# Kernel tuning notes

Measured on AMD Instinct MI355X. Metric: run time of the kernel, lower is better.

## Reference

```python
import jax, jax.numpy as jnp
import numpy as np

V, E, T, H, NT, B = 30000, 300, 256, 256, 9, 128


def setup_inputs() -> dict:
    key = jax.random.key(0)
    ks = jax.random.split(key, 12)
    s = 0.05
    # token ids with trailing zero padding (0 = pad), lens in [T//2, T]
    lens = jax.random.randint(ks[0], (B,), T // 2, T + 1)
    tokens = jax.random.randint(ks[1], (B, T), 1, V)
    pos = jnp.arange(T)[None, :]
    inputs = jnp.where(pos < lens[:, None], tokens, 0)
    labels = jax.random.randint(ks[2], (B, T), 0, NT)
    emb = jax.random.normal(ks[3], (V, E), jnp.float32) * s
    Wf = jax.random.normal(ks[4], (E, 4 * H), jnp.float32) * s
    Uf = jax.random.normal(ks[5], (H, 4 * H), jnp.float32) * s
    bf = jnp.zeros((4 * H,), jnp.float32)
    Wb = jax.random.normal(ks[6], (E, 4 * H), jnp.float32) * s
    Ub = jax.random.normal(ks[7], (H, 4 * H), jnp.float32) * s
    bb = jnp.zeros((4 * H,), jnp.float32)
    fcW = jax.random.normal(ks[8], (2 * H, NT), jnp.float32) * s
    fcb = jnp.zeros((NT,), jnp.float32)
    trans = jax.random.uniform(ks[9], (NT, NT), jnp.float32)  # tf.random.uniform init
    return dict(inputs=inputs, labels=labels, emb=emb, Wf=Wf, Uf=Uf, bf=bf,
                Wb=Wb, Ub=Ub, bb=bb, fcW=fcW, fcb=fcb, trans=trans)


def _lstm(x, W, U, b):
    """Keras LSTM (gate order i,f,g,o). x: [B,T,E] -> [B,T,H]."""
    xW = jnp.einsum('bte,eh->bth', x, W) + b  # precompute input projections

    def step(carry, xt):
        h, c = carry
        z = xt + h @ U
        i, f, g, o = jnp.split(z, 4, axis=-1)
        i = jax.nn.sigmoid(i)
        f = jax.nn.sigmoid(f)
        g = jnp.tanh(g)
        o = jax.nn.sigmoid(o)
        c = f * c + i * g
        h = o * jnp.tanh(c)
        return (h, c), h

    Bq = x.shape[0]
    Hq = U.shape[0]
    init = (jnp.zeros((Bq, Hq), x.dtype), jnp.zeros((Bq, Hq), x.dtype))
    _, hs = jax.lax.scan(step, init, jnp.swapaxes(xW, 0, 1))  # [T,B,H]
    return jnp.swapaxes(hs, 0, 1)


def _crf_log_likelihood(logits, labels, lens, trans):
    """tfa.text.crf_log_likelihood: gold score - log partition. logits: [B,T,N]."""
    Bq, Tq, Nq = logits.shape
    pos = jnp.arange(Tq)[None, :]
    mask = pos < lens[:, None]  # [B,T]
    # unary (emission) score of the gold path
    unary = jnp.take_along_axis(logits, labels[..., None], axis=-1)[..., 0]
    score = jnp.sum(jnp.where(mask, unary, 0.0), axis=-1)
    # binary (transition) score of the gold path
    btrans = trans[labels[:, :-1], labels[:, 1:]]
    bmask = pos[:, 1:] < lens[:, None]
    score = score + jnp.sum(jnp.where(bmask, btrans, 0.0), axis=-1)
    # forward algorithm (log partition) with per-timestep length masking
    def step(alpha, inp):
        logit_t, m_t = inp  # [B,N], [B]
        new = jax.nn.logsumexp(alpha[:, :, None] + trans[None], axis=1) + logit_t
        return jnp.where(m_t[:, None], new, alpha), None

    alpha0 = logits[:, 0]
    xs = (jnp.swapaxes(logits[:, 1:], 0, 1), jnp.swapaxes(mask[:, 1:], 0, 1))
    alpha, _ = jax.lax.scan(step, alpha0, xs)
    log_norm = jax.nn.logsumexp(alpha, axis=-1)
    return score - log_norm


def reference(inputs, labels, emb, Wf, Uf, bf, Wb, Ub, bb, fcW, fcb, trans):
    text_lens = jnp.sum((inputs != 0).astype(jnp.int32), axis=-1)
    x = emb[inputs]  # [B,T,E]
    hf = _lstm(x, Wf, Uf, bf)
    hb = _lstm(x[:, ::-1], Wb, Ub, bb)[:, ::-1]
    h = jnp.concatenate([hf, hb], axis=-1)  # [B,T,2H]
    logits = h @ fcW + fcb  # [B,T,NT]
    log_likelihood = _crf_log_likelihood(logits, labels, text_lens, trans)
    return logits, log_likelihood, text_lens
```

## Files before the change

kernel.cpp:

```cpp
#include <hip/hip_runtime.h>
#include <hip/hip_bf16.h>
#include <stdint.h>

#define Bb 128
#define Tt 256
#define Ee 300
#define EP 320
#define Hh 256
#define G4 1024
#define NTAG 9

typedef __bf16 bf16x8 __attribute__((ext_vector_type(8)));
typedef float f32x4 __attribute__((ext_vector_type(4)));
typedef float f32x2 __attribute__((ext_vector_type(2)));
typedef int i32x8 __attribute__((ext_vector_type(8)));
typedef unsigned short u16;
typedef unsigned int u32;
typedef unsigned char u8;
typedef long i64;

union U4B { uint4 q; bf16x8 v; };

static __device__ __forceinline__ float bf2f(u32 u){
  union { float f; u32 u; } w; w.u = u << 16; return w.f;
}
static __device__ __forceinline__ u16 f2bf(float f){
  union { float f; u32 u; } w; w.f = f;
  u32 x = w.u;
  return (u16)((x + 0x7fffu + ((x >> 16) & 1u)) >> 16);
}
static __device__ __forceinline__ int perm2orig(int c){
  int w = c >> 7, r = c & 127, g = r >> 5, jj = r & 31;
  return g * 256 + w * 32 + jj;
}
static __device__ __forceinline__ float frcp(float x){ return __builtin_amdgcn_rcpf(x); }
static __device__ __forceinline__ float fexp2(float x){
  float r; asm("v_exp_f32 %0, %1" : "=v"(r) : "v"(x)); return r;
}
static __device__ __forceinline__ f32x2 vexp2(f32x2 x){
  f32x2 r; r[0] = fexp2(x[0]); r[1] = fexp2(x[1]); return r;
}
static __device__ __forceinline__ f32x2 vrcp(f32x2 x){
  f32x2 r; r[0] = frcp(x[0]); r[1] = frcp(x[1]); return r;
}
static __device__ __forceinline__ f32x2 vfabs(f32x2 x){
  f32x2 r; r[0] = __builtin_fabsf(x[0]); r[1] = __builtin_fabsf(x[1]); return r;
}
static __device__ __forceinline__ f32x2 vminc(f32x2 x, float c){
  f32x2 r; r[0] = fminf(x[0], c); r[1] = fminf(x[1], c); return r;
}
static __device__ __forceinline__ f32x2 vcps(f32x2 m, f32x2 s){
  f32x2 r; r[0] = __builtin_copysignf(m[0], s[0]);
  r[1] = __builtin_copysignf(m[1], s[1]); return r;
}
static __device__ __forceinline__ void gl_lds16(const void* g, void* l){
  __builtin_amdgcn_global_load_lds((const __attribute__((address_space(1))) u32*)(g),
                                   (__attribute__((address_space(3))) u32*)(l), 16, 0, 0);
}

__global__ void pack_w_k(const float* __restrict__ Wf, const float* __restrict__ Wb,
                         u16* __restrict__ Wpk){
  int idx = blockIdx.x * 256 + threadIdx.x;
  if(idx >= 128 * 10 * 64) return;
  int lane = idx & 63;
  int kk = (idx >> 6) % 10;
  int nt2 = idx / 640;
  int d = nt2 >> 6, ntd = nt2 & 63;
  int oc = perm2orig(ntd * 16 + (lane & 15));
  const float* W = d ? Wb : Wf;
  int k0 = kk * 32 + ((lane >> 4) << 3);
  u16 o[8];
  #pragma unroll
  for(int j = 0; j < 8; ++j){
    int k = k0 + j;
    o[j] = (k < Ee) ? f2bf(W[(size_t)k * G4 + oc]) : (u16)0;
  }
  uint4 q;
  q.x = o[0] | ((u32)o[1] << 16); q.y = o[2] | ((u32)o[3] << 16);
  q.z = o[4] | ((u32)o[5] << 16); q.w = o[6] | ((u32)o[7] << 16);
  *(uint4*)(Wpk + (size_t)idx * 8) = q;
}

__global__ void pack_u_k(const float* __restrict__ Uf, const float* __restrict__ Ub,
                         u8* __restrict__ Upk8){
  int idx = blockIdx.x * 256 + threadIdx.x;
  if(idx >= 2 * 64 * 2 * 64) return;
  int lane = idx & 63;
  int kh = (idx >> 6) & 1;
  int nt = (idx >> 7) & 63;
  int d = idx >> 13;
  int oc = perm2orig(nt * 16 + (lane & 15));
  const float* U = d ? Ub : Uf;
  int k0 = kh * 128 + (lane >> 4) * 32;
  u32 o[8];
  #pragma unroll
  for(int m = 0; m < 8; ++m){
    float v0 = U[(size_t)(k0 + 4 * m + 0) * G4 + oc] * 32.f;
    float v1 = U[(size_t)(k0 + 4 * m + 1) * G4 + oc] * 32.f;
    float v2 = U[(size_t)(k0 + 4 * m + 2) * G4 + oc] * 32.f;
    float v3 = U[(size_t)(k0 + 4 * m + 3) * G4 + oc] * 32.f;
    int pk = __builtin_amdgcn_cvt_pk_fp8_f32(v0, v1, 0, false);
    pk = __builtin_amdgcn_cvt_pk_fp8_f32(v2, v3, pk, true);
    o[m] = (u32)pk;
  }
  uint4* dst = (uint4*)(Upk8 + (size_t)idx * 32);
  dst[0] = (uint4){o[0], o[1], o[2], o[3]};
  dst[1] = (uint4){o[4], o[5], o[6], o[7]};
}

__global__ void pack_b_k(const float* __restrict__ bf_, const float* __restrict__ bb_,
                         float* __restrict__ bperm){
  int c = blockIdx.x * 256 + threadIdx.x;
  if(c >= 2048) return;
  const float* src = (c >> 10) ? bb_ : bf_;
  bperm[c] = src[perm2orig(c & 1023)];
}

__global__ void pack_fcw_k(const float* __restrict__ fcW, u8* __restrict__ fcw8){
  int idx = blockIdx.x * 256 + threadIdx.x;
  if(idx >= 1024) return;
  int lane = idx & 63, kk = idx >> 6;
  int col = lane & 15;
  int k0 = kk * 32 + ((lane >> 4) << 3);
  float v[8];
  #pragma unroll
  for(int j = 0; j < 8; ++j)
    v[j] = (col < NTAG) ? fcW[(size_t)(k0 + j) * NTAG + col] * 256.f : 0.f;
  int lo = __builtin_amdgcn_cvt_pk_fp8_f32(v[0], v[1], 0, false);
  lo = __builtin_amdgcn_cvt_pk_fp8_f32(v[2], v[3], lo, true);
  int hi = __builtin_amdgcn_cvt_pk_fp8_f32(v[4], v[5], 0, false);
  hi = __builtin_amdgcn_cvt_pk_fp8_f32(v[6], v[7], hi, true);
  uint2 q; q.x = (u32)lo; q.y = (u32)hi;
  *(uint2*)(fcw8 + (size_t)idx * 8) = q;
}

__global__ void gather_x_k(const int* __restrict__ inp, const float* __restrict__ emb,
                           u16* __restrict__ xbf){
  int row = blockIdx.x * 2 + (threadIdx.x >> 7);
  int j = threadIdx.x & 127;
  int t = row >> 7, b = row & 127;
  int tok = inp[b * Tt + t];
  u16* dst = xbf + (size_t)row * EP;
  if(j < 75){
    float4 v = *(const float4*)(emb + (size_t)tok * Ee + j * 4);
    u32 lo = f2bf(v.x) | ((u32)f2bf(v.y) << 16);
    u32 hi = f2bf(v.z) | ((u32)f2bf(v.w) << 16);
    *(uint2*)(dst + j * 4) = (uint2){lo, hi};
  } else if(j < 80){
    *(uint2*)(dst + j * 4) = (uint2){0u, 0u};
  }
}

__global__ __launch_bounds__(256, 2) void xw_gemm_k(const u16* __restrict__ xbf,
    const u16* __restrict__ Wpk, const float* __restrict__ bperm,
    u16* __restrict__ xwpk){
  __shared__ uint4 At[512];
  int t = blockIdx.y, nblk = blockIdx.x;
  int tid = threadIdx.x, lane = tid & 63, w = tid >> 6;
  int mh = w >> 1, nh = w & 1;
  f32x4 acc[4][4];
  #pragma unroll
  for(int i = 0; i < 4; ++i)
    #pragma unroll
    for(int j = 0; j < 4; ++j) acc[i][j] = (f32x4){0.f, 0.f, 0.f, 0.f};
  for(int ks = 0; ks < 10; ++ks){
    __syncthreads();
    #pragma unroll
    for(int it = 0; it < 2; ++it){
      int row = it * 64 + w * 16 + (lane >> 2);
      int seg = (lane & 3) ^ (row & 3);
      gl_lds16(xbf + (size_t)(t * 128 + row) * EP + ks * 32 + seg * 8,
               &At[it * 256 + w * 64]);
    }
    asm volatile("s_waitcnt vmcnt(0)" ::: "memory");
    __syncthreads();
    U4B a[4], bv[4];
    #pragma unroll
    for(int m = 0; m < 4; ++m){
      int row = (mh * 4 + m) * 16 + (lane & 15);
      a[m].q = At[row * 4 + ((lane >> 4) ^ (row & 3))];
    }
    #pragma unroll
    for(int n = 0; n < 4; ++n){
      int ntg = nblk * 8 + nh * 4 + n;
      bv[n].q = *(const uint4*)(Wpk + ((size_t)(ntg * 10 + ks) * 64 + lane) * 8);
    }
    #pragma unroll
    for(int m = 0; m < 4; ++m)
      #pragma unroll
      for(int n = 0; n < 4; ++n)
        acc[m][n] = __builtin_amdgcn_mfma_f32_16x16x32_bf16(a[m].v, bv[n].v, acc[m][n], 0, 0, 0);
  }
  #pragma unroll
  for(int m = 0; m < 4; ++m){
    int grp = mh * 4 + m;
    #pragma unroll
    for(int n = 0; n < 4; ++n){
      int ntg = nblk * 8 + nh * 4 + n;
      int d = ntg >> 6, nd = ntg & 63;
      float bias = bperm[ntg * 16 + (lane & 15)];
      u16 h0 = f2bf((acc[m][n][0] + bias) * 512.f), h1 = f2bf((acc[m][n][1] + bias) * 512.f);
      u16 h2 = f2bf((acc[m][n][2] + bias) * 512.f), h3 = f2bf((acc[m][n][3] + bias) * 512.f);
      uint2 p; p.x = h0 | ((u32)h1 << 16); p.y = h2 | ((u32)h3 << 16);
      *(uint2*)(xwpk + ((((size_t)(d * 8 + grp) * Tt + t) * 64 + nd) * 64 + lane) * 4) = p;
    }
  }
}

__global__ __launch_bounds__(512, 2) void lstm_rec_k(const u16* __restrict__ xwpk,
    const u8* __restrict__ Upk8, u8* __restrict__ hseq8){
  __shared__ u32 Hf8[2][1024];
  __shared__ uint2 Xw[2][4096];
  int bid = blockIdx.x;
  int d = bid >> 3, grp = bid & 7;
  int tid = threadIdx.x, lane = tid & 63, w = tid >> 6;
  int arow = lane & 15, r4 = lane >> 4;
  if(w & 1) __builtin_amdgcn_s_setprio(1);

  i32x8 Ureg[8][2];
  const u8* Ub8 = Upk8 + (size_t)d * 262144;
  #pragma unroll
  for(int n = 0; n < 8; ++n)
    #pragma unroll
    for(int kh = 0; kh < 2; ++kh)
      Ureg[n][kh] = *(const i32x8*)(Ub8 + (((size_t)(w * 8 + n) * 2 + kh) * 64 + lane) * 32);
  #pragma unroll
  for(int n = 0; n < 8; ++n)
    #pragma unroll
    for(int kh = 0; kh < 2; ++kh)
      asm volatile("" : "+a"(Ureg[n][kh]));

  Hf8[0][tid] = 0u; Hf8[0][tid + 512] = 0u;
  f32x2 cst2[2][2];
  #pragma unroll
  for(int a = 0; a < 2; ++a)
    #pragma unroll
    for(int p = 0; p < 2; ++p) cst2[a][p] = (f32x2){0.f, 0.f};
  const u16* xwb = xwpk + (size_t)(d * 8 + grp) * Tt * 16384;
  u8* hs_base = hseq8 + (size_t)(d * 8 + grp) * Tt * 4096;
  u32 hf8base = (u32)(uintptr_t)(&Hf8[0][0]);
  u32* hf8u = (u32*)(&Hf8[0][0]);

  const float c1s = -1.44269504f / 512.f;
  const f32x2 C1  = (f32x2){c1s, c1s};
  const f32x2 C2  = (f32x2){2.f * c1s, 2.f * c1s};
  const f32x2 C3  = (f32x2){-2.f * 1.44269504f, -2.f * 1.44269504f};
  const f32x2 ONE = (f32x2){1.f, 1.f};

  {
    int t0 = d ? (Tt - 1) : 0;
    const u16* xwt0 = xwb + (size_t)t0 * 16384;
    #pragma unroll
    for(int j = 0; j < 4; ++j)
      gl_lds16(xwt0 + (w * 8 + 2 * j) * 256 + lane * 8, &Xw[0][w * 512 + 2 * j * 64]);
  }
  asm volatile("s_waitcnt vmcnt(0)" ::: "memory");
  __syncthreads();

  int cur = 0;
  for(int st = 0; st < Tt; ++st){
    int t = d ? (Tt - 1 - st) : st;
    int p = st & 1, c_ = p ^ 1;
    union AFU { i64 dd[4]; i32x8 v; };
    AFU af0, af1;
    u32 av = hf8base + (u32)(p * 4096) + (u32)(r4 * 512 + arow * 8);
    asm volatile("ds_read_b64_tr_b8 %0, %1"             : "=v"(af0.dd[0]) : "v"(av));
    asm volatile("ds_read_b64_tr_b8 %0, %1 offset:128"  : "=v"(af0.dd[1]) : "v"(av));
    asm volatile("ds_read_b64_tr_b8 %0, %1 offset:256"  : "=v"(af0.dd[2]) : "v"(av));
    asm volatile("ds_read_b64_tr_b8 %0, %1 offset:384"  : "=v"(af0.dd[3]) : "v"(av));
    asm volatile("ds_read_b64_tr_b8 %0, %1 offset:2048" : "=v"(af1.dd[0]) : "v"(av));
    asm volatile("ds_read_b64_tr_b8 %0, %1 offset:2176" : "=v"(af1.dd[1]) : "v"(av));
    asm volatile("ds_read_b64_tr_b8 %0, %1 offset:2304" : "=v"(af1.dd[2]) : "v"(av));
    asm volatile("ds_read_b64_tr_b8 %0, %1 offset:2432" : "=v"(af1.dd[3]) : "v"(av));
    asm volatile("s_waitcnt lgkmcnt(0)" ::: "memory");
    __builtin_amdgcn_sched_barrier(0);
    asm volatile("s_waitcnt vmcnt(2)" ::: "memory");
    uint2 xw[8];
    #pragma unroll
    for(int n = 0; n < 8; ++n) xw[n] = Xw[cur][w * 512 + n * 64 + lane];
    {
      int stn = (st + 1 < Tt) ? st + 1 : st;
      int tn = d ? (Tt - 1 - stn) : stn;
      const u16* xwtn = xwb + (size_t)tn * 16384;
      #pragma unroll
      for(int j = 0; j < 4; ++j)
        gl_lds16(xwtn + (w * 8 + 2 * j) * 256 + lane * 8, &Xw[cur ^ 1][w * 512 + 2 * j * 64]);
    }
    __builtin_amdgcn_sched_barrier(0);
    f32x4 acc[8];
    #pragma unroll
    for(int n = 0; n < 8; ++n){
      acc[n][0] = bf2f(xw[n].x & 0xffffu);
      acc[n][1] = bf2f(xw[n].x >> 16);
      acc[n][2] = bf2f(xw[n].y & 0xffffu);
      acc[n][3] = bf2f(xw[n].y >> 16);
    }
    #pragma unroll
    for(int n = 0; n < 8; ++n){
      asm volatile("v_mfma_f32_16x16x128_f8f6f4 %0, %1, %2, %0"
                   : "+v"(acc[n]) : "v"(af0.v), "a"(Ureg[n][0]));
      asm volatile("v_mfma_f32_16x16x128_f8f6f4 %0, %1, %2, %0"
                   : "+v"(acc[n]) : "v"(af1.v), "a"(Ureg[n][1]));
    }
    #pragma unroll
    for(int n1 = 0; n1 < 2; ++n1){
      f32x2 h16[2];
      #pragma unroll
      for(int pq = 0; pq < 2; ++pq){
        f32x2 ai = (f32x2){acc[0 + n1][2 * pq], acc[0 + n1][2 * pq + 1]};
        f32x2 af = (f32x2){acc[2 + n1][2 * pq], acc[2 + n1][2 * pq + 1]};
        f32x2 ag = (f32x2){acc[4 + n1][2 * pq], acc[4 + n1][2 * pq + 1]};
        f32x2 ao = (f32x2){acc[6 + n1][2 * pq], acc[6 + n1][2 * pq + 1]};
        f32x2 ei = vexp2(ai * C1);
        f32x2 ef = vexp2(af * C1);
        f32x2 eo = vexp2(ao * C1);
        f32x2 eg = vexp2(vminc(vfabs(ag), 10240.f) * C2);
        f32x2 ig = vcps(ONE - eg, ag) * vrcp((ONE + ei) * (ONE + eg));
        f32x2 fs = vrcp(ONE + ef);
        f32x2 cc = fs * cst2[n1][pq] + ig;
        cst2[n1][pq] = cc;
        f32x2 ec = vexp2(vminc(vfabs(cc), 20.f) * C3);
        f32x2 hh = vcps(ONE - ec, cc) * vrcp((ONE + eo) * (ONE + ec));
        h16[pq] = hh * (f32x2){16.f, 16.f};
      }
      int pk = __builtin_amdgcn_cvt_pk_fp8_f32(h16[0][0], h16[0][1], 0, false);
      pk = __builtin_amdgcn_cvt_pk_fp8_f32(h16[1][0], h16[1][1], pk, true);
      int unit = w * 32 + n1 * 16 + arow;
      hf8u[c_ * 1024 + unit * 4 + r4] = (u32)pk;
      *(u32*)(hs_base + (size_t)t * 4096 + unit * 16 + r4 * 4) = (u32)pk;
    }
    asm volatile("s_waitcnt lgkmcnt(0)" ::: "memory");
    __builtin_amdgcn_s_barrier();
    cur ^= 1;
  }
}

__global__ __launch_bounds__(256) void logits_k(const u8* __restrict__ hseq8,
    const u8* __restrict__ fcw8, const float* __restrict__ fcb,
    float* __restrict__ out){
  __shared__ u8 Ht[4][8192];
  int widx = threadIdx.x >> 6, lane = threadIdx.x & 63;
  int wid = blockIdx.x * 4 + widx;
  int grp = wid >> 8, t = wid & 255;
  i64 bf[16];
  #pragma unroll
  for(int kk = 0; kk < 16; ++kk)
    bf[kk] = *(const i64*)(fcw8 + ((size_t)kk * 64 + lane) * 8);
  const u8* hf = hseq8 + ((size_t)(0 * 8 + grp) * Tt + t) * 4096;
  const u8* hb = hseq8 + ((size_t)(1 * 8 + grp) * Tt + t) * 4096;
  #pragma unroll
  for(int j = 0; j < 4; ++j){
    gl_lds16(hf + j * 1024 + lane * 16, &Ht[widx][j * 1024]);
    gl_lds16(hb + j * 1024 + lane * 16, &Ht[widx][4096 + j * 1024]);
  }
  asm volatile("s_waitcnt vmcnt(0)" ::: "memory");
  __builtin_amdgcn_sched_barrier(0);
  u32 base = (u32)(uintptr_t)(&Ht[widx][0]) + lane * 8;
  i64 afr[16];
  #pragma unroll
  for(int kk = 0; kk < 16; ++kk){
    u32 a = base + kk * 512;
    asm volatile("ds_read_b64_tr_b8 %0, %1" : "=v"(afr[kk]) : "v"(a));
  }
  asm volatile("s_waitcnt lgkmcnt(0)" ::: "memory");
  __builtin_amdgcn_sched_barrier(0);
  f32x4 acc = (f32x4){0.f, 0.f, 0.f, 0.f};
  #pragma unroll
  for(int kk = 0; kk < 16; ++kk)
    acc = __builtin_amdgcn_mfma_f32_16x16x32_fp8_fp8(afr[kk], bf[kk], acc, 0, 0, 0);
  int tag = lane & 15, r4 = lane >> 4;
  if(tag < NTAG){
    float bb = fcb[tag];
    #pragma unroll
    for(int q = 0; q < 4; ++q){
      int b = grp * 16 + r4 * 4 + q;
      out[((size_t)b * Tt + t) * NTAG + tag] = acc[q] * (1.f / 4096.f) + bb;
    }
  }
}

__global__ __launch_bounds__(64) void crf_k(const int* __restrict__ inp,
    const int* __restrict__ labels, const float* __restrict__ trans,
    const float* __restrict__ logits, float* __restrict__ out){
  int b = blockIdx.x;
  int lane = threadIdx.x;
  int cnt = 0;
  for(int t = lane; t < Tt; t += 64) cnt += (inp[b * Tt + t] != 0) ? 1 : 0;
  #pragma unroll
  for(int off = 32; off >= 1; off >>= 1) cnt += __shfl_xor(cnt, off, 64);
  int len = cnt;
  float sc = 0.f;
  for(int t = lane; t < Tt; t += 64){
    if(t < len){
      int lab = labels[b * Tt + t];
      sc += logits[(size_t)(b * Tt + t) * NTAG + lab];
      if(t >= 1){
        int lp = labels[b * Tt + t - 1];
        sc += trans[lp * NTAG + lab];
      }
    }
  }
  #pragma unroll
  for(int off = 32; off >= 1; off >>= 1) sc += __shfl_xor(sc, off, 64);
  float Tc[NTAG];
  if(lane < NTAG){
    #pragma unroll
    for(int i = 0; i < NTAG; ++i) Tc[i] = trans[i * NTAG + lane];
  }
  float alpha = (lane < NTAG) ? logits[(size_t)(b * Tt) * NTAG + lane] : -3.0e38f;
  for(int t = 1; t < len; ++t){
    float av[NTAG];
    #pragma unroll
    for(int i = 0; i < NTAG; ++i) av[i] = __shfl(alpha, i, 64);
    if(lane < NTAG){
      float m = av[0] + Tc[0];
      #pragma unroll
      for(int i = 1; i < NTAG; ++i) m = fmaxf(m, av[i] + Tc[i]);
      float s = 0.f;
      #pragma unroll
      for(int i = 0; i < NTAG; ++i) s += __expf(av[i] + Tc[i] - m);
      alpha = __logf(s) + m + logits[(size_t)(b * Tt + t) * NTAG + lane];
    }
  }
  float av[NTAG];
  #pragma unroll
  for(int i = 0; i < NTAG; ++i) av[i] = __shfl(alpha, i, 64);
  float m = av[0];
  #pragma unroll
  for(int i = 1; i < NTAG; ++i) m = fmaxf(m, av[i]);
  float s = 0.f;
  #pragma unroll
  for(int i = 0; i < NTAG; ++i) s += __expf(av[i] - m);
  float ln = __logf(s) + m;
  if(lane == 0){
    out[(size_t)Bb * Tt * NTAG + b] = sc - ln;
    out[(size_t)Bb * Tt * NTAG + Bb + b] = (float)len;
  }
}

extern "C" void kernel_launch(void* const* d_in, const int* in_sizes, int n_in,
                              void* d_out, int out_size, void* d_ws, size_t ws_size,
                              hipStream_t stream) {
  const int*   inputs = (const int*)d_in[0];
  const int*   labels = (const int*)d_in[1];
  const float* emb    = (const float*)d_in[2];
  const float* Wf     = (const float*)d_in[3];
  const float* Uf     = (const float*)d_in[4];
  const float* bf_    = (const float*)d_in[5];
  const float* Wb     = (const float*)d_in[6];
  const float* Ub     = (const float*)d_in[7];
  const float* bb_    = (const float*)d_in[8];
  const float* fcW    = (const float*)d_in[9];
  const float* fcb    = (const float*)d_in[10];
  const float* trans  = (const float*)d_in[11];
  float* out = (float*)d_out;
  char* ws = (char*)d_ws;
  u16*   xwpk  = (u16*)(ws + 0);
  u8*    hseq8 = (u8*) (ws + 134217728);
  u8*    Upk8  = (u8*) (ws + 150994944);
  u16*   Wpk   = (u16*)(ws + 151519232);
  float* bperm = (float*)(ws + 152829952);
  u8*    fcw8  = (u8*) (ws + 152838144);
  u16*   xbf   = (u16*)(ws + 152846336);

  hipLaunchKernelGGL(pack_w_k, dim3(320), dim3(256), 0, stream, Wf, Wb, Wpk);
  hipLaunchKernelGGL(pack_u_k, dim3(64), dim3(256), 0, stream, Uf, Ub, Upk8);
  hipLaunchKernelGGL(pack_b_k, dim3(8), dim3(256), 0, stream, bf_, bb_, bperm);
  hipLaunchKernelGGL(pack_fcw_k, dim3(4), dim3(256), 0, stream, fcW, fcw8);
  hipLaunchKernelGGL(gather_x_k, dim3(16384), dim3(256), 0, stream, inputs, emb, xbf);
  hipLaunchKernelGGL(xw_gemm_k, dim3(16, 256), dim3(256), 0, stream, xbf, Wpk, bperm, xwpk);
  hipLaunchKernelGGL(lstm_rec_k, dim3(16), dim3(512), 0, stream, xwpk, Upk8, hseq8);
  hipLaunchKernelGGL(logits_k, dim3(512), dim3(256), 0, stream, hseq8, fcw8, fcb, out);
  hipLaunchKernelGGL(crf_k, dim3(128), dim3(64), 0, stream, inputs, labels, trans, out, out);
}
```

Measured before the change: 582.2 us.

## Merge pack kernels into one launch, process two timesteps per GEMM block, drop setprio

Folds the four weight/bias packing kernels into a single prep kernel dispatched by block index, which removes three kernel launches. The input-projection GEMM now has each block handle two timesteps, so the packed W fragments loaded per k-step feed twice as many MFMAs and the grid shrinks by half. Separately, the recurrent LSTM kernel no longer raises priority for odd waves. The GEMM change doubles accumulator registers and LDS use per block, which may lower occupancy.

```diff
diff --git a/kernel.cpp b/kernel.cpp
--- a/kernel.cpp
+++ b/kernel.cpp
@@ -58,80 +58,79 @@
                                    (__attribute__((address_space(3))) u32*)(l), 16, 0, 0);
 }
 
-__global__ void pack_w_k(const float* __restrict__ Wf, const float* __restrict__ Wb,
-                         u16* __restrict__ Wpk){
-  int idx = blockIdx.x * 256 + threadIdx.x;
-  if(idx >= 128 * 10 * 64) return;
-  int lane = idx & 63;
-  int kk = (idx >> 6) % 10;
-  int nt2 = idx / 640;
-  int d = nt2 >> 6, ntd = nt2 & 63;
-  int oc = perm2orig(ntd * 16 + (lane & 15));
-  const float* W = d ? Wb : Wf;
-  int k0 = kk * 32 + ((lane >> 4) << 3);
-  u16 o[8];
-  #pragma unroll
-  for(int j = 0; j < 8; ++j){
-    int k = k0 + j;
-    o[j] = (k < Ee) ? f2bf(W[(size_t)k * G4 + oc]) : (u16)0;
-  }
-  uint4 q;
-  q.x = o[0] | ((u32)o[1] << 16); q.y = o[2] | ((u32)o[3] << 16);
-  q.z = o[4] | ((u32)o[5] << 16); q.w = o[6] | ((u32)o[7] << 16);
-  *(uint4*)(Wpk + (size_t)idx * 8) = q;
-}
-
-__global__ void pack_u_k(const float* __restrict__ Uf, const float* __restrict__ Ub,
-                         u8* __restrict__ Upk8){
-  int idx = blockIdx.x * 256 + threadIdx.x;
-  if(idx >= 2 * 64 * 2 * 64) return;
-  int lane = idx & 63;
-  int kh = (idx >> 6) & 1;
-  int nt = (idx >> 7) & 63;
-  int d = idx >> 13;
-  int oc = perm2orig(nt * 16 + (lane & 15));
-  const float* U = d ? Ub : Uf;
-  int k0 = kh * 128 + (lane >> 4) * 32;
-  u32 o[8];
-  #pragma unroll
-  for(int m = 0; m < 8; ++m){
-    float v0 = U[(size_t)(k0 + 4 * m + 0) * G4 + oc] * 32.f;
-    float v1 = U[(size_t)(k0 + 4 * m + 1) * G4 + oc] * 32.f;
-    float v2 = U[(size_t)(k0 + 4 * m + 2) * G4 + oc] * 32.f;
-    float v3 = U[(size_t)(k0 + 4 * m + 3) * G4 + oc] * 32.f;
-    int pk = __builtin_amdgcn_cvt_pk_fp8_f32(v0, v1, 0, false);
-    pk = __builtin_amdgcn_cvt_pk_fp8_f32(v2, v3, pk, true);
-    o[m] = (u32)pk;
-  }
-  uint4* dst = (uint4*)(Upk8 + (size_t)idx * 32);
-  dst[0] = (uint4){o[0], o[1], o[2], o[3]};
-  dst[1] = (uint4){o[4], o[5], o[6], o[7]};
-}
-
-__global__ void pack_b_k(const float* __restrict__ bf_, const float* __restrict__ bb_,
-                         float* __restrict__ bperm){
-  int c = blockIdx.x * 256 + threadIdx.x;
-  if(c >= 2048) return;
-  const float* src = (c >> 10) ? bb_ : bf_;
-  bperm[c] = src[perm2orig(c & 1023)];
-}
-
-__global__ void pack_fcw_k(const float* __restrict__ fcW, u8* __restrict__ fcw8){
-  int idx = blockIdx.x * 256 + threadIdx.x;
-  if(idx >= 1024) return;
-  int lane = idx & 63, kk = idx >> 6;
-  int col = lane & 15;
-  int k0 = kk * 32 + ((lane >> 4) << 3);
-  float v[8];
-  #pragma unroll
-  for(int j = 0; j < 8; ++j)
-    v[j] = (col < NTAG) ? fcW[(size_t)(k0 + j) * NTAG + col] * 256.f : 0.f;
-  int lo = __builtin_amdgcn_cvt_pk_fp8_f32(v[0], v[1], 0, false);
-  lo = __builtin_amdgcn_cvt_pk_fp8_f32(v[2], v[3], lo, true);
-  int hi = __builtin_amdgcn_cvt_pk_fp8_f32(v[4], v[5], 0, false);
-  hi = __builtin_amdgcn_cvt_pk_fp8_f32(v[6], v[7], hi, true);
-  uint2 q; q.x = (u32)lo; q.y = (u32)hi;
-  *(uint2*)(fcw8 + (size_t)idx * 8) = q;
+__global__ void prep_k(const float* __restrict__ Wf, const float* __restrict__ Wb,
+                       const float* __restrict__ Uf, const float* __restrict__ Ub,
+                       const float* __restrict__ bf_, const float* __restrict__ bb_,
+                       const float* __restrict__ fcW,
+                       u16* __restrict__ Wpk, u8* __restrict__ Upk8,
+                       float* __restrict__ bperm, u8* __restrict__ fcw8){
+  int blk = blockIdx.x;
+  if(blk < 320){
+    int idx = blk * 256 + threadIdx.x;
+    if(idx >= 128 * 10 * 64) return;
+    int lane = idx & 63;
+    int kk = (idx >> 6) % 10;
+    int nt2 = idx / 640;
+    int d = nt2 >> 6, ntd = nt2 & 63;
+    int oc = perm2orig(ntd * 16 + (lane & 15));
+    const float* W = d ? Wb : Wf;
+    int k0 = kk * 32 + ((lane >> 4) << 3);
+    u16 o[8];
+    #pragma unroll
+    for(int j = 0; j < 8; ++j){
+      int k = k0 + j;
+      o[j] = (k < Ee) ? f2bf(W[(size_t)k * G4 + oc]) : (u16)0;
+    }
+    uint4 q;
+    q.x = o[0] | ((u32)o[1] << 16); q.y = o[2] | ((u32)o[3] << 16);
+    q.z = o[4] | ((u32)o[5] << 16); q.w = o[6] | ((u32)o[7] << 16);
+    *(uint4*)(Wpk + (size_t)idx * 8) = q;
+  } else if(blk < 384){
+    int idx = (blk - 320) * 256 + threadIdx.x;
+    if(idx >= 2 * 64 * 2 * 64) return;
+    int lane = idx & 63;
+    int kh = (idx >> 6) & 1;
+    int nt = (idx >> 7) & 63;
+    int d = idx >> 13;
+    int oc = perm2orig(nt * 16 + (lane & 15));
+    const float* U = d ? Ub : Uf;
+    int k0 = kh * 128 + (lane >> 4) * 32;
+    u32 o[8];
+    #pragma unroll
+    for(int m = 0; m < 8; ++m){
+      float v0 = U[(size_t)(k0 + 4 * m + 0) * G4 + oc] * 32.f;
+      float v1 = U[(size_t)(k0 + 4 * m + 1) * G4 + oc] * 32.f;
+      float v2 = U[(size_t)(k0 + 4 * m + 2) * G4 + oc] * 32.f;
+      float v3 = U[(size_t)(k0 + 4 * m + 3) * G4 + oc] * 32.f;
+      int pk = __builtin_amdgcn_cvt_pk_fp8_f32(v0, v1, 0, false);
+      pk = __builtin_amdgcn_cvt_pk_fp8_f32(v2, v3, pk, true);
+      o[m] = (u32)pk;
+    }
+    uint4* dst = (uint4*)(Upk8 + (size_t)idx * 32);
+    dst[0] = (uint4){o[0], o[1], o[2], o[3]};
+    dst[1] = (uint4){o[4], o[5], o[6], o[7]};
+  } else if(blk < 392){
+    int c = (blk - 384) * 256 + threadIdx.x;
+    if(c >= 2048) return;
+    const float* src = (c >> 10) ? bb_ : bf_;
+    bperm[c] = src[perm2orig(c & 1023)];
+  } else {
+    int idx = (blk - 392) * 256 + threadIdx.x;
+    if(idx >= 1024) return;
+    int lane = idx & 63, kk = idx >> 6;
+    int col = lane & 15;
+    int k0 = kk * 32 + ((lane >> 4) << 3);
+    float v[8];
+    #pragma unroll
+    for(int j = 0; j < 8; ++j)
+      v[j] = (col < NTAG) ? fcW[(size_t)(k0 + j) * NTAG + col] * 256.f : 0.f;
+    int lo = __builtin_amdgcn_cvt_pk_fp8_f32(v[0], v[1], 0, false);
+    lo = __builtin_amdgcn_cvt_pk_fp8_f32(v[2], v[3], lo, true);
+    int hi = __builtin_amdgcn_cvt_pk_fp8_f32(v[4], v[5], 0, false);
+    hi = __builtin_amdgcn_cvt_pk_fp8_f32(v[6], v[7], hi, true);
+    uint2 q; q.x = (u32)lo; q.y = (u32)hi;
+    *(uint2*)(fcw8 + (size_t)idx * 8) = q;
+  }
 }
 
 __global__ void gather_x_k(const int* __restrict__ inp, const float* __restrict__ emb,
@@ -154,55 +153,67 @@
 __global__ __launch_bounds__(256, 2) void xw_gemm_k(const u16* __restrict__ xbf,
     const u16* __restrict__ Wpk, const float* __restrict__ bperm,
     u16* __restrict__ xwpk){
-  __shared__ uint4 At[512];
-  int t = blockIdx.y, nblk = blockIdx.x;
+  __shared__ uint4 At[2][512];
+  int t0 = blockIdx.y * 2, nblk = blockIdx.x;
   int tid = threadIdx.x, lane = tid & 63, w = tid >> 6;
   int mh = w >> 1, nh = w & 1;
-  f32x4 acc[4][4];
-  #pragma unroll
-  for(int i = 0; i < 4; ++i)
-    #pragma unroll
-    for(int j = 0; j < 4; ++j) acc[i][j] = (f32x4){0.f, 0.f, 0.f, 0.f};
+  f32x4 acc[2][4][4];
+  #pragma unroll
+  for(int tt = 0; tt < 2; ++tt)
+    #pragma unroll
+    for(int i = 0; i < 4; ++i)
+      #pragma unroll
+      for(int j = 0; j < 4; ++j) acc[tt][i][j] = (f32x4){0.f, 0.f, 0.f, 0.f};
   for(int ks = 0; ks < 10; ++ks){
     __syncthreads();
     #pragma unroll
     for(int it = 0; it < 2; ++it){
       int row = it * 64 + w * 16 + (lane >> 2);
       int seg = (lane & 3) ^ (row & 3);
-      gl_lds16(xbf + (size_t)(t * 128 + row) * EP + ks * 32 + seg * 8,
-               &At[it * 256 + w * 64]);
+      gl_lds16(xbf + (size_t)(t0 * 128 + row) * EP + ks * 32 + seg * 8,
+               &At[0][it * 256 + w * 64]);
+      gl_lds16(xbf + (size_t)((t0 + 1) * 128 + row) * EP + ks * 32 + seg * 8,
+               &At[1][it * 256 + w * 64]);
     }
     asm volatile("s_waitcnt vmcnt(0)" ::: "memory");
     __syncthreads();
-    U4B a[4], bv[4];
-    #pragma unroll
-    for(int m = 0; m < 4; ++m){
-      int row = (mh * 4 + m) * 16 + (lane & 15);
-      a[m].q = At[row * 4 + ((lane >> 4) ^ (row & 3))];
-    }
+    U4B bv[4];
     #pragma unroll
     for(int n = 0; n < 4; ++n){
       int ntg = nblk * 8 + nh * 4 + n;
       bv[n].q = *(const uint4*)(Wpk + ((size_t)(ntg * 10 + ks) * 64 + lane) * 8);
     }
     #pragma unroll
-    for(int m = 0; m < 4; ++m)
-      #pragma unroll
-      for(int n = 0; n < 4; ++n)
-        acc[m][n] = __builtin_amdgcn_mfma_f32_16x16x32_bf16(a[m].v, bv[n].v, acc[m][n], 0, 0, 0);
-  }
-  #pragma unroll
-  for(int m = 0; m < 4; ++m){
-    int grp = mh * 4 + m;
-    #pragma unroll
-    for(int n = 0; n < 4; ++n){
-      int ntg = nblk * 8 + nh * 4 + n;
-      int d = ntg >> 6, nd = ntg & 63;
-      float bias = bperm[ntg * 16 + (lane & 15)];
-      u16 h0 = f2bf((acc[m][n][0] + bias) * 512.f), h1 = f2bf((acc[m][n][1] + bias) * 512.f);
-      u16 h2 = f2bf((acc[m][n][2] + bias) * 512.f), h3 = f2bf((acc[m][n][3] + bias) * 512.f);
-      uint2 p; p.x = h0 | ((u32)h1 << 16); p.y = h2 | ((u32)h3 << 16);
-      *(uint2*)(xwpk + ((((size_t)(d * 8 + grp) * Tt + t) * 64 + nd) * 64 + lane) * 4) = p;
+    for(int tt = 0; tt < 2; ++tt){
+      U4B a[4];
+      #pragma unroll
+      for(int m = 0; m < 4; ++m){
+        int row = (mh * 4 + m) * 16 + (lane & 15);
+        a[m].q = At[tt][row * 4 + ((lane >> 4) ^ (row & 3))];
+      }
+      #pragma unroll
+      for(int m = 0; m < 4; ++m)
+        #pragma unroll
+        for(int n = 0; n < 4; ++n)
+          acc[tt][m][n] = __builtin_amdgcn_mfma_f32_16x16x32_bf16(a[m].v, bv[n].v, acc[tt][m][n], 0, 0, 0);
+    }
+  }
+  #pragma unroll
+  for(int tt = 0; tt < 2; ++tt){
+    int t = t0 + tt;
+    #pragma unroll
+    for(int m = 0; m < 4; ++m){
+      int grp = mh * 4 + m;
+      #pragma unroll
+      for(int n = 0; n < 4; ++n){
+        int ntg = nblk * 8 + nh * 4 + n;
+        int d = ntg >> 6, nd = ntg & 63;
+        float bias = bperm[ntg * 16 + (lane & 15)];
+        u16 h0 = f2bf((acc[tt][m][n][0] + bias) * 512.f), h1 = f2bf((acc[tt][m][n][1] + bias) * 512.f);
+        u16 h2 = f2bf((acc[tt][m][n][2] + bias) * 512.f), h3 = f2bf((acc[tt][m][n][3] + bias) * 512.f);
+        uint2 p; p.x = h0 | ((u32)h1 << 16); p.y = h2 | ((u32)h3 << 16);
+        *(uint2*)(xwpk + ((((size_t)(d * 8 + grp) * Tt + t) * 64 + nd) * 64 + lane) * 4) = p;
+      }
     }
   }
 }
@@ -215,7 +226,6 @@
   int d = bid >> 3, grp = bid & 7;
   int tid = threadIdx.x, lane = tid & 63, w = tid >> 6;
   int arow = lane & 15, r4 = lane >> 4;
-  if(w & 1) __builtin_amdgcn_s_setprio(1);
 
   i32x8 Ureg[8][2];
   const u8* Ub8 = Upk8 + (size_t)d * 262144;
@@ -463,12 +473,10 @@
   u8*    fcw8  = (u8*) (ws + 152838144);
   u16*   xbf   = (u16*)(ws + 152846336);
 
-  hipLaunchKernelGGL(pack_w_k, dim3(320), dim3(256), 0, stream, Wf, Wb, Wpk);
-  hipLaunchKernelGGL(pack_u_k, dim3(64), dim3(256), 0, stream, Uf, Ub, Upk8);
-  hipLaunchKernelGGL(pack_b_k, dim3(8), dim3(256), 0, stream, bf_, bb_, bperm);
-  hipLaunchKernelGGL(pack_fcw_k, dim3(4), dim3(256), 0, stream, fcW, fcw8);
+  hipLaunchKernelGGL(prep_k, dim3(396), dim3(256), 0, stream,
+                     Wf, Wb, Uf, Ub, bf_, bb_, fcW, Wpk, Upk8, bperm, fcw8);
   hipLaunchKernelGGL(gather_x_k, dim3(16384), dim3(256), 0, stream, inputs, emb, xbf);
-  hipLaunchKernelGGL(xw_gemm_k, dim3(16, 256), dim3(256), 0, stream, xbf, Wpk, bperm, xwpk);
+  hipLaunchKernelGGL(xw_gemm_k, dim3(16, 128), dim3(256), 0, stream, xbf, Wpk, bperm, xwpk);
   hipLaunchKernelGGL(lstm_rec_k, dim3(16), dim3(512), 0, stream, xwpk, Upk8, hseq8);
   hipLaunchKernelGGL(logits_k, dim3(512), dim3(256), 0, stream, hseq8, fcw8, fcb, out);
   hipLaunchKernelGGL(crf_k, dim3(128), dim3(64), 0, stream, inputs, labels, trans, out, out);
```

Result: no change. 580.0 us (-0.4%).
